# Kernel tuning notes

Measured on AMD Instinct MI355X. Metric: run time of the kernel, lower is better.

The kernel has to match this reference:

```python
import jax, jax.numpy as jnp
from jax import lax
import numpy as np

SPAN_WIDTH = 10


def setup_inputs() -> dict:
    key = jax.random.key(0)
    ks = jax.random.split(key, 8)
    B, S, H, E, L = 1, 512, 768, 1024, 50
    return {
        "hidden_states": jax.random.normal(ks[0], (B, S, H), jnp.float32),
        "gcn_W": jax.random.normal(ks[1], (L, H, H), jnp.float32) * 0.02,
        "gcn_b": jnp.zeros((L, H), jnp.float32),
        "attn_w": jax.random.normal(ks[2], (H,), jnp.float32) * 0.02,
        "attn_b": jnp.zeros((), jnp.float32),
        "ms_W1": jax.random.normal(ks[3], (3 * H, 3 * H), jnp.float32) * 0.02,
        "ms_b1": jnp.zeros((3 * H,), jnp.float32),
        "ms_W2": jax.random.normal(ks[4], (3 * H,), jnp.float32) * 0.02,
        "ms_b2": jnp.zeros((), jnp.float32),
        "edge_src": jax.random.randint(ks[5], (B, E), 0, S, jnp.int32),
        "edge_tgt": jax.random.randint(ks[6], (B, E), 0, S, jnp.int32),
        "edge_label": jax.random.randint(ks[7], (B, E), 0, L, jnp.int32),
    }


def _span_index_tables(S):
    # all candidate spans (i, j) with i <= j < min(i + SPAN_WIDTH, S); static given S
    starts, ends = [], []
    for i in range(S):
        for j in range(i, min(i + SPAN_WIDTH, S)):
            starts.append(i)
            ends.append(j)
    starts = np.asarray(starts, np.int32)
    ends = np.asarray(ends, np.int32)
    offs = np.arange(SPAN_WIDTH, dtype=np.int32)
    pos = np.minimum(starts[:, None] + offs, S - 1)        # [Ns, W] clamped gather idx
    mask = (starts[:, None] + offs) <= ends[:, None]       # [Ns, W] valid-token mask
    return starts, ends, pos, mask


def reference(hidden_states, gcn_W, gcn_b, attn_w, attn_b,
              ms_W1, ms_b1, ms_W2, ms_b2,
              edge_src, edge_tgt, edge_label):
    B, S, H = hidden_states.shape
    L = gcn_W.shape[0]
    batch_ix = jnp.arange(B)[:, None]                      # [B, 1]

    # ---- GCN layer: gather source nodes, per-label linear, scatter-add to targets ----
    x_src = hidden_states[batch_ix, edge_src]              # [B, E, H]

    def step(acc, inp):
        Wl, bl, l = inp
        y = x_src @ Wl + bl                                # [B, E, H]
        acc = acc + jnp.where((edge_label == l)[..., None], y, jnp.zeros_like(y))
        return acc, None

    acc0 = jnp.zeros_like(x_src)
    msgs, _ = lax.scan(step, acc0, (gcn_W, gcn_b, jnp.arange(L, dtype=edge_label.dtype)))
    gcn_out = jnp.zeros_like(hidden_states).at[batch_ix, edge_tgt].add(msgs)
    gcn_out = jax.nn.relu(gcn_out)

    # combine_strategy == 'add'
    emb = hidden_states + gcn_out                          # [B, S, H]

    # ---- span representation: attention pooling over each candidate span ----
    starts, ends, pos, mask = _span_index_tables(S)
    span_tok = emb[:, pos]                                 # [B, Ns, W, H]
    scores = jnp.einsum('bnwh,h->bnw', span_tok, attn_w) + attn_b
    scores = jnp.where(mask[None], scores, -jnp.inf)
    wts = jax.nn.softmax(scores, axis=-1)                  # softmax over span tokens
    attn_out = jnp.einsum('bnw,bnwh->bnh', wts, span_tok)  # [B, Ns, H]
    span_vec = jnp.concatenate([emb[:, starts], emb[:, ends], attn_out], axis=-1)  # [B, Ns, 3H]

    # ---- mention scorer: Linear(3H,3H) -> ReLU -> Linear(3H,1) ----
    hdn = jax.nn.relu(span_vec @ ms_W1 + ms_b1)
    mention_scores = hdn @ ms_W2 + ms_b2                   # [B, Ns]
    return mention_scores
```

## Files before the change

### kernel.cpp

```cpp
#include <hip/hip_runtime.h>

#define S_ 512
#define H_ 768
#define E_ 1024
#define L_ 50
#define NSPAN 5075
#define K3H 2304

typedef __attribute__((ext_vector_type(8))) short short8;
typedef __attribute__((ext_vector_type(4))) float f32x4;

__device__ __forceinline__ ushort f2bf(float f) {
  uint u = __float_as_uint(f);
  u += 0x7fffu + ((u >> 16) & 1u);
  return (ushort)(u >> 16);
}
__device__ __forceinline__ float bf2f(ushort u) {
  return __uint_as_float(((uint)u) << 16);
}

__global__ void k_bin(const int* __restrict__ lbl, int* __restrict__ loff,
                      int* __restrict__ esort) {
  __shared__ int cnt[L_], cur[L_];
  int t = threadIdx.x;
  if (t < L_) cnt[t] = 0;
  __syncthreads();
  for (int e = t; e < E_; e += 256) atomicAdd(&cnt[lbl[e]], 1);
  __syncthreads();
  if (t == 0) {
    int s = 0;
    for (int l = 0; l < L_; ++l) { loff[l] = s; cur[l] = s; s += cnt[l]; }
    loff[L_] = s;
  }
  __syncthreads();
  for (int e = t; e < E_; e += 256) {
    int sl = atomicAdd(&cur[lbl[e]], 1);
    esort[sl] = e;
  }
}

__global__ __launch_bounds__(256) void k_gcn3(
    const float* __restrict__ hidden, const float* __restrict__ gW,
    const float* __restrict__ gb, const int* __restrict__ esrc,
    const int* __restrict__ etgt, const int* __restrict__ loff,
    const int* __restrict__ esort, float* __restrict__ gout) {
  int l = blockIdx.x, cb = blockIdx.y;
  int t = threadIdx.x;
  int o0 = loff[l], ne = loff[l + 1] - o0;
  if (ne == 0) return;
  __shared__ short xs[2048];
  __shared__ short Ws[8192];
  __shared__ int src_s[32], tgt_s[32];
  int lane = t & 63, w = t >> 6;
  int c0 = cb * 128;
  int j = t & 127, hoct = t >> 7;
  const float* Wbase = gW + (size_t)l * H_ * H_ + c0 + j;
  int sm = t & 31, soct = t >> 5;

  for (int m0 = 0; m0 < ne; m0 += 32) {
    int nc = min(32, ne - m0);
    __syncthreads();
    if (t < 32) {
      int ed = esort[o0 + m0 + ((t < nc) ? t : 0)];
      src_s[t] = esrc[ed];
      tgt_s[t] = etgt[ed];
    }
    __syncthreads();
    f32x4 acc[2][2];
#pragma unroll
    for (int mf = 0; mf < 2; ++mf)
#pragma unroll
      for (int nf = 0; nf < 2; ++nf) acc[mf][nf] = (f32x4){0.f, 0.f, 0.f, 0.f};
    const float* xrow = hidden + (size_t)src_s[sm] * H_ + soct * 8;
    bool xvalid = sm < nc;

    for (int k0 = 0; k0 < H_; k0 += 64) {
      __syncthreads();
      short8 xv = {0, 0, 0, 0, 0, 0, 0, 0};
      if (xvalid) {
        float4 x0 = *(const float4*)(xrow + k0);
        float4 x1 = *(const float4*)(xrow + k0 + 4);
        xv[0] = (short)f2bf(x0.x); xv[1] = (short)f2bf(x0.y);
        xv[2] = (short)f2bf(x0.z); xv[3] = (short)f2bf(x0.w);
        xv[4] = (short)f2bf(x1.x); xv[5] = (short)f2bf(x1.y);
        xv[6] = (short)f2bf(x1.z); xv[7] = (short)f2bf(x1.w);
      }
      *(short8*)&xs[(soct * 32 + sm) * 8] = xv;
#pragma unroll
      for (int p = 0; p < 4; ++p) {
        int io = p * 2 + hoct;
        const float* wp = Wbase + (size_t)(k0 + io * 8) * H_;
        short8 wv;
#pragma unroll
        for (int q = 0; q < 8; ++q) wv[q] = (short)f2bf(wp[(size_t)q * H_]);
        *(short8*)&Ws[(io * 128 + j) * 8] = wv;
      }
      __syncthreads();
#pragma unroll
      for (int ks = 0; ks < 2; ++ks) {
        int kg = ks * 4 + (lane >> 4);
        short8 af[2], bfv[2];
#pragma unroll
        for (int mf = 0; mf < 2; ++mf)
          af[mf] = *(const short8*)&xs[(kg * 32 + mf * 16 + (lane & 15)) * 8];
#pragma unroll
        for (int nf = 0; nf < 2; ++nf)
          bfv[nf] = *(const short8*)&Ws[(kg * 128 + w * 32 + nf * 16 + (lane & 15)) * 8];
#pragma unroll
        for (int mf = 0; mf < 2; ++mf)
#pragma unroll
          for (int nf = 0; nf < 2; ++nf)
            acc[mf][nf] = __builtin_amdgcn_mfma_f32_16x16x32_bf16(af[mf], bfv[nf], acc[mf][nf], 0, 0, 0);
      }
    }
#pragma unroll
    for (int mf = 0; mf < 2; ++mf) {
      int e0 = mf * 16 + (lane >> 4) * 4;
#pragma unroll
      for (int nf = 0; nf < 2; ++nf) {
        int col = c0 + w * 32 + nf * 16 + (lane & 15);
        float bias = gb[l * H_ + col];
#pragma unroll
        for (int reg = 0; reg < 4; ++reg) {
          int e = e0 + reg;
          if (e < nc)
            atomicAdd(&gout[(size_t)tgt_s[e] * H_ + col], acc[mf][nf][reg] + bias);
        }
      }
    }
  }
}

__global__ void k_emb(const float* __restrict__ hidden, const float* __restrict__ gout,
                      const float* __restrict__ aw, ushort* __restrict__ emb_b,
                      float* __restrict__ tsc) {
  int p = blockIdx.x, t = threadIdx.x;
  float dot = 0.f;
#pragma unroll
  for (int c = 0; c < 3; ++c) {
    int h = t + c * 256;
    float g = gout[(size_t)p * H_ + h];
    float v = hidden[(size_t)p * H_ + h] + fmaxf(g, 0.f);
    emb_b[(size_t)p * H_ + h] = f2bf(v);
    dot += v * aw[h];
  }
#pragma unroll
  for (int off = 32; off; off >>= 1) dot += __shfl_down(dot, off);
  __shared__ float red[4];
  if ((t & 63) == 0) red[t >> 6] = dot;
  __syncthreads();
  if (t == 0) tsc[p] = red[0] + red[1] + red[2] + red[3];
}

__global__ __launch_bounds__(256) void k_pgemm(
    const ushort* __restrict__ emb_b, const float* __restrict__ W1,
    ushort* __restrict__ P) {
  __shared__ short As[8192];
  __shared__ short Bs[8192];
  int t = threadIdx.x;
  int lane = t & 63, w = t >> 6;
  int m0 = blockIdx.x * 128, c0 = blockIdx.y * 128, seg = blockIdx.z;
  int wr = w >> 1, wc = w & 1;
  const ushort* pa = emb_b + (size_t)(m0 + (t & 127)) * H_ + (t >> 7) * 8;
  short* ldsA = &As[w * 512];
  int j = t & 127, hoct = t >> 7;
  const float* Wb = W1 + (size_t)(seg * H_) * K3H + c0 + j;

  f32x4 acc[4][4];
#pragma unroll
  for (int mf = 0; mf < 4; ++mf)
#pragma unroll
    for (int nf = 0; nf < 4; ++nf) acc[mf][nf] = (f32x4){0.f, 0.f, 0.f, 0.f};

  for (int k0 = 0; k0 < H_; k0 += 64) {
    __syncthreads();
#pragma unroll
    for (int i = 0; i < 4; ++i)
      __builtin_amdgcn_global_load_lds((const uint*)(pa + k0 + i * 16),
                                       (uint*)(ldsA + i * 2048), 16, 0, 0);
#pragma unroll
    for (int p = 0; p < 4; ++p) {
      int io = p * 2 + hoct;
      const float* wp = Wb + (size_t)(k0 + io * 8) * K3H;
      short8 wv;
#pragma unroll
      for (int q = 0; q < 8; ++q) wv[q] = (short)f2bf(wp[(size_t)q * K3H]);
      *(short8*)&Bs[(io * 128 + j) * 8] = wv;
    }
    __syncthreads();
#pragma unroll
    for (int ks = 0; ks < 2; ++ks) {
      int kg = ks * 4 + (lane >> 4);
      int rbase = (kg * 128 + wr * 64 + (lane & 15)) * 8;
      int cbase = (kg * 128 + wc * 64 + (lane & 15)) * 8;
      short8 af[4], bfv[4];
#pragma unroll
      for (int mf = 0; mf < 4; ++mf) af[mf] = *(const short8*)&As[rbase + mf * 128];
#pragma unroll
      for (int nf = 0; nf < 4; ++nf) bfv[nf] = *(const short8*)&Bs[cbase + nf * 128];
#pragma unroll
      for (int mf = 0; mf < 4; ++mf)
#pragma unroll
        for (int nf = 0; nf < 4; ++nf)
          acc[mf][nf] = __builtin_amdgcn_mfma_f32_16x16x32_bf16(af[mf], bfv[nf], acc[mf][nf], 0, 0, 0);
    }
  }
  ushort* Pseg = P + (size_t)seg * S_ * K3H;
#pragma unroll
  for (int mf = 0; mf < 4; ++mf)
#pragma unroll
    for (int nf = 0; nf < 4; ++nf) {
      int col = c0 + wc * 64 + nf * 16 + (lane & 15);
#pragma unroll
      for (int reg = 0; reg < 4; ++reg) {
        int m = m0 + wr * 64 + mf * 16 + ((lane >> 4) << 2) + reg;
        Pseg[(size_t)m * K3H + col] = f2bf(acc[mf][nf][reg]);
      }
    }
}

__global__ __launch_bounds__(256) void k_span(
    const ushort* __restrict__ P, const float* __restrict__ tsc,
    const float* __restrict__ b1, const float* __restrict__ W2,
    const float* __restrict__ b2, float* __restrict__ out) {
  __shared__ short Ps[3 * 13 * 768];
  __shared__ float tss[13];
  int t = threadIdx.x;
  int i0 = blockIdx.x * 4;
  int ct = blockIdx.y, cc0 = ct * 768;
  for (int idx = t; idx < 3744; idx += 256) {
    int mat = idx / 1248;
    int rem = idx - mat * 1248;
    int r = rem / 96, part = rem - r * 96;
    int row = min(i0 + r, S_ - 1);
    short8 v = *(const short8*)(P + (size_t)mat * S_ * K3H + (size_t)row * K3H + cc0 + part * 8);
    *(short8*)&Ps[idx * 8] = v;
  }
  if (t < 13) tss[t] = tsc[min(i0 + t, S_ - 1)];
  __syncthreads();

  int w = t >> 6, lane = t & 63;
  int i = i0 + w;
  int maxlen = min(10, S_ - i);
  int base = (i <= 502) ? 10 * i : NSPAN - (S_ - i) * (S_ + 1 - i) / 2;

  float p1r[12], b1r[12], w2r[12];
#pragma unroll
  for (int jj = 0; jj < 12; ++jj) {
    int c = lane + 64 * jj;
    p1r[jj] = bf2f((ushort)Ps[0 * 9984 + w * 768 + c]);
    b1r[jj] = b1[cc0 + c];
    w2r[jj] = W2[cc0 + c];
  }
  float bias2 = (ct == 0) ? b2[0] : 0.f;

  for (int L = 1; L <= maxlen; ++L) {
    float wts[10];
    float mx = -1e30f;
    for (int q = 0; q < L; ++q) mx = fmaxf(mx, tss[w + q]);
    float s = 0.f;
    for (int q = 0; q < L; ++q) { wts[q] = __expf(tss[w + q] - mx); s += wts[q]; }
    float inv = 1.f / s;

    float part = 0.f;
#pragma unroll
    for (int jj = 0; jj < 12; ++jj) {
      int c = lane + 64 * jj;
      float a = 0.f;
      for (int q = 0; q < L; ++q)
        a = fmaf(wts[q], bf2f((ushort)Ps[2 * 9984 + (w + q) * 768 + c]), a);
      float v = p1r[jj] + bf2f((ushort)Ps[1 * 9984 + (w + L - 1) * 768 + c]) + b1r[jj] + a * inv;
      part = fmaf(fmaxf(v, 0.f), w2r[jj], part);
    }
#pragma unroll
    for (int off = 32; off; off >>= 1) part += __shfl_xor(part, off);
    if (lane == 0) atomicAdd(&out[base + L - 1], part + bias2);
  }
}

extern "C" void kernel_launch(void* const* d_in, const int* in_sizes, int n_in,
                              void* d_out, int out_size, void* d_ws, size_t ws_size,
                              hipStream_t stream) {
  const float* hidden = (const float*)d_in[0];
  const float* gW     = (const float*)d_in[1];
  const float* gb     = (const float*)d_in[2];
  const float* aw     = (const float*)d_in[3];
  const float* W1     = (const float*)d_in[5];
  const float* b1     = (const float*)d_in[6];
  const float* W2     = (const float*)d_in[7];
  const float* b2     = (const float*)d_in[8];
  const int* esrc     = (const int*)d_in[9];
  const int* etgt     = (const int*)d_in[10];
  const int* elbl     = (const int*)d_in[11];
  float* out = (float*)d_out;

  float* ws     = (float*)d_ws;
  float* gout   = ws;
  float* tsc    = gout + S_ * H_;
  ushort* emb_b = (ushort*)(tsc + 512);
  ushort* P     = emb_b + (size_t)S_ * H_;
  int* loff     = (int*)(P + (size_t)3 * S_ * K3H);
  int* esort    = loff + 64;

  hipMemsetAsync(gout, 0, S_ * H_ * sizeof(float), stream);
  hipMemsetAsync(d_out, 0, (size_t)out_size * sizeof(float), stream);
  k_bin<<<1, 256, 0, stream>>>(elbl, loff, esort);
  k_gcn3<<<dim3(L_, 6), 256, 0, stream>>>(hidden, gW, gb, esrc, etgt, loff, esort, gout);
  k_emb<<<S_, 256, 0, stream>>>(hidden, gout, aw, emb_b, tsc);
  k_pgemm<<<dim3(4, 18, 3), 256, 0, stream>>>(emb_b, W1, P);
  k_span<<<dim3(128, 3), 256, 0, stream>>>(P, tsc, b1, W2, b2, out);
}
```

Measured before the change: 297.5 us.

## Prepack W1 to bf16 tiles, split GCN K, shrink pgemm tiles, incremental span softmax

Adds a kernel that converts W1 to bf16 and stores it in MFMA tile order, so the projection GEMM can fill shared memory with direct global-to-LDS loads instead of strided fp32 loads plus conversion. The GCN kernel is split over two K halves to double the grid, with the bias added only by the first half. The pgemm M tile is halved to launch more blocks. The span kernel now uses smaller blocks and computes the softmax-weighted sum incrementally across span lengths, which removes the quadratic inner loop. The costs are an extra pack pass over W1 on every call and more atomics in the GCN.

```diff
diff --git a/kernel.cpp b/kernel.cpp
--- a/kernel.cpp
+++ b/kernel.cpp
@@ -39,12 +39,29 @@
   }
 }
 
+__global__ void k_bpack(const float* __restrict__ W1, ushort* __restrict__ Bp) {
+  int nblk = blockIdx.x, kstep = blockIdx.y;
+  int t = threadIdx.x;
+  int col = t & 127, kg2 = t >> 7;
+  const float* src = W1 + (size_t)(kstep * 64) * K3H + nblk * 128 + col;
+  ushort* dst = Bp + (size_t)(nblk * 36 + kstep) * 8192;
+#pragma unroll
+  for (int g = 0; g < 4; ++g) {
+    int kgrp = kg2 * 4 + g;
+    short8 pv;
+#pragma unroll
+    for (int e = 0; e < 8; ++e)
+      pv[e] = (short)f2bf(src[(size_t)(kgrp * 8 + e) * K3H]);
+    *(short8*)(dst + (size_t)kgrp * 1024 + col * 8) = pv;
+  }
+}
+
 __global__ __launch_bounds__(256) void k_gcn3(
     const float* __restrict__ hidden, const float* __restrict__ gW,
     const float* __restrict__ gb, const int* __restrict__ esrc,
     const int* __restrict__ etgt, const int* __restrict__ loff,
     const int* __restrict__ esort, float* __restrict__ gout) {
-  int l = blockIdx.x, cb = blockIdx.y;
+  int l = blockIdx.x, cb = blockIdx.y, kb = blockIdx.z;
   int t = threadIdx.x;
   int o0 = loff[l], ne = loff[l + 1] - o0;
   if (ne == 0) return;
@@ -56,6 +73,7 @@
   int j = t & 127, hoct = t >> 7;
   const float* Wbase = gW + (size_t)l * H_ * H_ + c0 + j;
   int sm = t & 31, soct = t >> 5;
+  int kbeg = kb * 384, kend = kbeg + 384;
 
   for (int m0 = 0; m0 < ne; m0 += 32) {
     int nc = min(32, ne - m0);
@@ -74,7 +92,7 @@
     const float* xrow = hidden + (size_t)src_s[sm] * H_ + soct * 8;
     bool xvalid = sm < nc;
 
-    for (int k0 = 0; k0 < H_; k0 += 64) {
+    for (int k0 = kbeg; k0 < kend; k0 += 64) {
       __syncthreads();
       short8 xv = {0, 0, 0, 0, 0, 0, 0, 0};
       if (xvalid) {
@@ -119,7 +137,7 @@
 #pragma unroll
       for (int nf = 0; nf < 2; ++nf) {
         int col = c0 + w * 32 + nf * 16 + (lane & 15);
-        float bias = gb[l * H_ + col];
+        float bias = (kb == 0) ? gb[l * H_ + col] : 0.f;
 #pragma unroll
         for (int reg = 0; reg < 4; ++reg) {
           int e = e0 + reg;
@@ -153,53 +171,48 @@
 }
 
 __global__ __launch_bounds__(256) void k_pgemm(
-    const ushort* __restrict__ emb_b, const float* __restrict__ W1,
+    const ushort* __restrict__ emb_b, const ushort* __restrict__ Bp,
     ushort* __restrict__ P) {
-  __shared__ short As[8192];
+  __shared__ short As[4096];
   __shared__ short Bs[8192];
   int t = threadIdx.x;
   int lane = t & 63, w = t >> 6;
-  int m0 = blockIdx.x * 128, c0 = blockIdx.y * 128, seg = blockIdx.z;
+  int m0 = blockIdx.x * 64, c0 = blockIdx.y * 128, seg = blockIdx.z;
   int wr = w >> 1, wc = w & 1;
-  const ushort* pa = emb_b + (size_t)(m0 + (t & 127)) * H_ + (t >> 7) * 8;
-  short* ldsA = &As[w * 512];
-  int j = t & 127, hoct = t >> 7;
-  const float* Wb = W1 + (size_t)(seg * H_) * K3H + c0 + j;
-
-  f32x4 acc[4][4];
-#pragma unroll
-  for (int mf = 0; mf < 4; ++mf)
+  const ushort* pa = emb_b + (size_t)(m0 + lane) * H_;
+  const ushort* pb = Bp + ((size_t)blockIdx.y * 36 + seg * 12) * 8192 + t * 8;
+
+  f32x4 acc[2][4];
+#pragma unroll
+  for (int mf = 0; mf < 2; ++mf)
 #pragma unroll
     for (int nf = 0; nf < 4; ++nf) acc[mf][nf] = (f32x4){0.f, 0.f, 0.f, 0.f};
 
-  for (int k0 = 0; k0 < H_; k0 += 64) {
+  for (int kk = 0; kk < 12; ++kk) {
+    int k0 = kk * 64;
     __syncthreads();
 #pragma unroll
+    for (int i = 0; i < 2; ++i)
+      __builtin_amdgcn_global_load_lds((const uint*)(pa + k0 + (w + i * 4) * 8),
+                                       (uint*)&As[(w + i * 4) * 512], 16, 0, 0);
+#pragma unroll
     for (int i = 0; i < 4; ++i)
-      __builtin_amdgcn_global_load_lds((const uint*)(pa + k0 + i * 16),
-                                       (uint*)(ldsA + i * 2048), 16, 0, 0);
-#pragma unroll
-    for (int p = 0; p < 4; ++p) {
-      int io = p * 2 + hoct;
-      const float* wp = Wb + (size_t)(k0 + io * 8) * K3H;
-      short8 wv;
-#pragma unroll
-      for (int q = 0; q < 8; ++q) wv[q] = (short)f2bf(wp[(size_t)q * K3H]);
-      *(short8*)&Bs[(io * 128 + j) * 8] = wv;
-    }
+      __builtin_amdgcn_global_load_lds((const uint*)(pb + (size_t)kk * 8192 + i * 2048),
+                                       (uint*)&Bs[w * 512 + i * 2048], 16, 0, 0);
     __syncthreads();
+
 #pragma unroll
     for (int ks = 0; ks < 2; ++ks) {
       int kg = ks * 4 + (lane >> 4);
-      int rbase = (kg * 128 + wr * 64 + (lane & 15)) * 8;
+      int rbase = (kg * 64 + wr * 32 + (lane & 15)) * 8;
       int cbase = (kg * 128 + wc * 64 + (lane & 15)) * 8;
-      short8 af[4], bfv[4];
-#pragma unroll
-      for (int mf = 0; mf < 4; ++mf) af[mf] = *(const short8*)&As[rbase + mf * 128];
+      short8 af[2], bfv[4];
+#pragma unroll
+      for (int mf = 0; mf < 2; ++mf) af[mf] = *(const short8*)&As[rbase + mf * 128];
 #pragma unroll
       for (int nf = 0; nf < 4; ++nf) bfv[nf] = *(const short8*)&Bs[cbase + nf * 128];
 #pragma unroll
-      for (int mf = 0; mf < 4; ++mf)
+      for (int mf = 0; mf < 2; ++mf)
 #pragma unroll
         for (int nf = 0; nf < 4; ++nf)
           acc[mf][nf] = __builtin_amdgcn_mfma_f32_16x16x32_bf16(af[mf], bfv[nf], acc[mf][nf], 0, 0, 0);
@@ -207,13 +220,13 @@
   }
   ushort* Pseg = P + (size_t)seg * S_ * K3H;
 #pragma unroll
-  for (int mf = 0; mf < 4; ++mf)
+  for (int mf = 0; mf < 2; ++mf)
 #pragma unroll
     for (int nf = 0; nf < 4; ++nf) {
       int col = c0 + wc * 64 + nf * 16 + (lane & 15);
 #pragma unroll
       for (int reg = 0; reg < 4; ++reg) {
-        int m = m0 + wr * 64 + mf * 16 + ((lane >> 4) << 2) + reg;
+        int m = m0 + wr * 32 + mf * 16 + ((lane >> 4) << 2) + reg;
         Pseg[(size_t)m * K3H + col] = f2bf(acc[mf][nf][reg]);
       }
     }
@@ -223,55 +236,62 @@
     const ushort* __restrict__ P, const float* __restrict__ tsc,
     const float* __restrict__ b1, const float* __restrict__ W2,
     const float* __restrict__ b2, float* __restrict__ out) {
-  __shared__ short Ps[3 * 13 * 768];
-  __shared__ float tss[13];
-  int t = threadIdx.x;
-  int i0 = blockIdx.x * 4;
-  int ct = blockIdx.y, cc0 = ct * 768;
-  for (int idx = t; idx < 3744; idx += 256) {
-    int mat = idx / 1248;
-    int rem = idx - mat * 1248;
-    int r = rem / 96, part = rem - r * 96;
+  __shared__ short Ps[3][11][384];
+  __shared__ float tss[11];
+  int t = threadIdx.x;
+  int i0 = blockIdx.x * 2;
+  int ct = blockIdx.y, cc0 = ct * 384;
+  for (int idx = t; idx < 1584; idx += 256) {
+    int mat = idx / 528;
+    int rem = idx - mat * 528;
+    int r = rem / 48, part = rem - r * 48;
     int row = min(i0 + r, S_ - 1);
-    short8 v = *(const short8*)(P + (size_t)mat * S_ * K3H + (size_t)row * K3H + cc0 + part * 8);
-    *(short8*)&Ps[idx * 8] = v;
-  }
-  if (t < 13) tss[t] = tsc[min(i0 + t, S_ - 1)];
+    short8 v = *(const short8*)(P + ((size_t)mat * S_ + row) * K3H + cc0 + part * 8);
+    *(short8*)&Ps[mat][r][part * 8] = v;
+  }
+  if (t < 11) tss[t] = tsc[min(i0 + t, S_ - 1)];
   __syncthreads();
 
   int w = t >> 6, lane = t & 63;
-  int i = i0 + w;
+  int sl = w >> 1, ch = w & 1;
+  int i = i0 + sl;
   int maxlen = min(10, S_ - i);
   int base = (i <= 502) ? 10 * i : NSPAN - (S_ - i) * (S_ + 1 - i) / 2;
 
-  float p1r[12], b1r[12], w2r[12];
-#pragma unroll
-  for (int jj = 0; jj < 12; ++jj) {
-    int c = lane + 64 * jj;
-    p1r[jj] = bf2f((ushort)Ps[0 * 9984 + w * 768 + c]);
-    b1r[jj] = b1[cc0 + c];
-    w2r[jj] = W2[cc0 + c];
-  }
-  float bias2 = (ct == 0) ? b2[0] : 0.f;
-
-  for (int L = 1; L <= maxlen; ++L) {
-    float wts[10];
-    float mx = -1e30f;
-    for (int q = 0; q < L; ++q) mx = fmaxf(mx, tss[w + q]);
-    float s = 0.f;
-    for (int q = 0; q < L; ++q) { wts[q] = __expf(tss[w + q] - mx); s += wts[q]; }
-    float inv = 1.f / s;
-
-    float part = 0.f;
-#pragma unroll
-    for (int jj = 0; jj < 12; ++jj) {
-      int c = lane + 64 * jj;
-      float a = 0.f;
-      for (int q = 0; q < L; ++q)
-        a = fmaf(wts[q], bf2f((ushort)Ps[2 * 9984 + (w + q) * 768 + c]), a);
-      float v = p1r[jj] + bf2f((ushort)Ps[1 * 9984 + (w + L - 1) * 768 + c]) + b1r[jj] + a * inv;
-      part = fmaf(fmaxf(v, 0.f), w2r[jj], part);
-    }
+  int ca = ch * 192 + lane, cb2 = ca + 64, cc2 = ca + 128;
+  float p10 = bf2f((ushort)Ps[0][sl][ca]);
+  float p11 = bf2f((ushort)Ps[0][sl][cb2]);
+  float p12 = bf2f((ushort)Ps[0][sl][cc2]);
+  float b10 = b1[cc0 + ca], b11 = b1[cc0 + cb2], b12 = b1[cc0 + cc2];
+  float w20 = W2[cc0 + ca], w21 = W2[cc0 + cb2], w22 = W2[cc0 + cc2];
+  float bias2 = (ct == 0 && ch == 0) ? b2[0] : 0.f;
+
+  float mx = -1e30f;
+#pragma unroll
+  for (int q = 0; q < 10; ++q)
+    if (q < maxlen) mx = fmaxf(mx, tss[sl + q]);
+  float e[10];
+#pragma unroll
+  for (int q = 0; q < 10; ++q)
+    e[q] = (q < maxlen) ? __expf(tss[sl + q] - mx) : 0.f;
+
+  float A0 = 0.f, A1 = 0.f, A2 = 0.f, Ssum = 0.f;
+#pragma unroll
+  for (int L = 1; L <= 10; ++L) {
+    if (L > maxlen) break;
+    int r = sl + L - 1;
+    float ee = e[L - 1];
+    Ssum += ee;
+    float inv = 1.f / Ssum;
+    A0 = fmaf(ee, bf2f((ushort)Ps[2][r][ca]), A0);
+    A1 = fmaf(ee, bf2f((ushort)Ps[2][r][cb2]), A1);
+    A2 = fmaf(ee, bf2f((ushort)Ps[2][r][cc2]), A2);
+    float v0 = p10 + bf2f((ushort)Ps[1][r][ca]) + b10 + A0 * inv;
+    float v1 = p11 + bf2f((ushort)Ps[1][r][cb2]) + b11 + A1 * inv;
+    float v2 = p12 + bf2f((ushort)Ps[1][r][cc2]) + b12 + A2 * inv;
+    float part = fmaf(fmaxf(v0, 0.f), w20, 0.f);
+    part = fmaf(fmaxf(v1, 0.f), w21, part);
+    part = fmaf(fmaxf(v2, 0.f), w22, part);
 #pragma unroll
     for (int off = 32; off; off >>= 1) part += __shfl_xor(part, off);
     if (lane == 0) atomicAdd(&out[base + L - 1], part + bias2);
@@ -299,14 +319,16 @@
   float* tsc    = gout + S_ * H_;
   ushort* emb_b = (ushort*)(tsc + 512);
   ushort* P     = emb_b + (size_t)S_ * H_;
-  int* loff     = (int*)(P + (size_t)3 * S_ * K3H);
+  ushort* Bp    = P + (size_t)3 * S_ * K3H;
+  int* loff     = (int*)(Bp + (size_t)K3H * K3H);
   int* esort    = loff + 64;
 
   hipMemsetAsync(gout, 0, S_ * H_ * sizeof(float), stream);
   hipMemsetAsync(d_out, 0, (size_t)out_size * sizeof(float), stream);
   k_bin<<<1, 256, 0, stream>>>(elbl, loff, esort);
-  k_gcn3<<<dim3(L_, 6), 256, 0, stream>>>(hidden, gW, gb, esrc, etgt, loff, esort, gout);
+  k_bpack<<<dim3(18, 36), 256, 0, stream>>>(W1, Bp);
+  k_gcn3<<<dim3(L_, 6, 2), 256, 0, stream>>>(hidden, gW, gb, esrc, etgt, loff, esort, gout);
   k_emb<<<S_, 256, 0, stream>>>(hidden, gout, aw, emb_b, tsc);
-  k_pgemm<<<dim3(4, 18, 3), 256, 0, stream>>>(emb_b, W1, P);
-  k_span<<<dim3(128, 3), 256, 0, stream>>>(P, tsc, b1, W2, b2, out);
-}
+  k_pgemm<<<dim3(8, 18, 3), 256, 0, stream>>>(emb_b, Bp, P);
+  k_span<<<dim3(256, 6), 256, 0, stream>>>(P, tsc, b1, W2, b2, out);
+}
```

After: 263.9 us. -11.3%, faster.
